# Optimization experiments

Hardware: AMD Instinct MI355X
Metric: run time of the kernel (lower is better)

Reference implementation:

```python
import jax, jax.numpy as jnp
import numpy as np

B, C, NQ, NK, S, H, FF = 8, 256, 1024, 4096, 16, 8, 2048
DH = C // H
EPS = 1e-5


def _layernorm(x, g, b):
    m = jnp.mean(x, axis=-1, keepdims=True)
    v = jnp.mean((x - m) ** 2, axis=-1, keepdims=True)
    return (x - m) * jax.lax.rsqrt(v + EPS) * g + b


def _box_query(key_pos, query_pos):
    # key_pos: (B,NK,3); query_pos: (B,NQ,6) = centers ++ box sizes (L,H,W)
    centers = query_pos[:, :, None, :3]            # (B,NQ,1,3)
    half = 0.5 * query_pos[:, :, None, 3:]         # (B,NQ,1,3)
    off = jnp.abs(key_pos[:, None, :, :] - centers)  # (B,NQ,NK,3)
    inside = jnp.all(off <= half, axis=-1)         # (B,NQ,NK)
    # first n_sample inside-points in index order (stable sort: inside first)
    order = jnp.argsort(~inside, axis=-1, stable=True)
    idx = order[..., :S]                           # (B,NQ,S)
    valid = jnp.take_along_axis(inside, idx, axis=-1)
    mask = ~valid                                  # True = padded / masked
    idx = jnp.where(mask, 0, idx)
    mask = mask.at[..., 0].set(False)              # matches cuda path: slot 0 never masked
    return idx, mask


def _forward(query, key, query_pos, key_pos,
             q_w, q_b, k_w, k_b, v_w, v_b, o_w, o_b,
             lin1_w, lin1_b, lin2_w, lin2_b,
             n1_g, n1_b, n2_g, n2_b, qpe_w, qpe_b, kpe_w, kpe_b):
    idx, mask = _box_query(key_pos, query_pos)     # (B,NQ,S), (B,NQ,S)
    # gather neighborhoods
    gxyz = jax.vmap(lambda kp, ix: kp[ix])(key_pos, idx)        # (B,NQ,S,3)
    gxyz = gxyz - query_pos[:, :, None, :3]                     # center-relative
    gfeat = jax.vmap(lambda kf, ix: kf[:, ix])(key, idx)        # (B,C,NQ,S)

    BQ = B * NQ
    kfeat = jnp.transpose(gfeat, (0, 2, 3, 1)).reshape(BQ, S, C)   # (BQ,S,C)
    kpe = gxyz.reshape(BQ, S, 3) @ kpe_w.T + kpe_b                 # cross_embed
    qtok = jnp.transpose(query, (0, 2, 1)).reshape(BQ, C)          # (BQ,C)
    qpe = (query_pos @ qpe_w.T + qpe_b).reshape(BQ, C)             # pos_embed

    # multihead cross-attention: 1 query vs S=16 local keys per group
    kv_in = kfeat + kpe
    qh = ((qtok + qpe) @ q_w.T + q_b).reshape(BQ, H, DH)
    kh = (kv_in @ k_w.T + k_b).reshape(BQ, S, H, DH)
    vh = (kv_in @ v_w.T + v_b).reshape(BQ, S, H, DH)
    scores = jnp.einsum('bhd,bshd->bhs', qh, kh) / np.sqrt(DH)    # (BQ,H,S)
    scores = jnp.where(mask.reshape(BQ, 1, S), -1e30, scores)
    attn = jax.nn.softmax(scores, axis=-1)
    ao = jnp.einsum('bhs,bshd->bhd', attn, vh).reshape(BQ, C)
    ao = ao @ o_w.T + o_b

    x = _layernorm(qtok + ao, n1_g, n1_b)                         # post-norm
    ff = jax.nn.relu(x @ lin1_w.T + lin1_b) @ lin2_w.T + lin2_b
    x = _layernorm(x + ff, n2_g, n2_b)
    return jnp.transpose(x.reshape(B, NQ, C), (0, 2, 1))          # (B,C,NQ)


def setup_inputs() -> dict:
    rng = jax.random.key(0)
    ks = jax.random.split(rng, 24)
    s = 0.02
    query = jax.random.normal(ks[0], (B, C, NQ), jnp.float32)
    key = jax.random.normal(ks[1], (B, C, NK), jnp.float32)
    key_pos = jax.random.uniform(ks[2], (B, NK, 3), jnp.float32)
    centers = jax.random.uniform(ks[3], (B, NQ, 3), jnp.float32)
    sizes = jax.random.uniform(ks[4], (B, NQ, 3), jnp.float32, minval=0.1, maxval=0.4)
    query_pos = jnp.concatenate([centers, sizes], axis=-1)
    p = {
        'q_w': jax.random.normal(ks[5], (C, C)) * s, 'q_b': jnp.zeros((C,)),
        'k_w': jax.random.normal(ks[6], (C, C)) * s, 'k_b': jnp.zeros((C,)),
        'v_w': jax.random.normal(ks[7], (C, C)) * s, 'v_b': jnp.zeros((C,)),
        'o_w': jax.random.normal(ks[8], (C, C)) * s, 'o_b': jnp.zeros((C,)),
        'lin1_w': jax.random.normal(ks[9], (FF, C)) * s, 'lin1_b': jnp.zeros((FF,)),
        'lin2_w': jax.random.normal(ks[10], (C, FF)) * s, 'lin2_b': jnp.zeros((C,)),
        'n1_g': jnp.ones((C,)), 'n1_b': jnp.zeros((C,)),
        'n2_g': jnp.ones((C,)), 'n2_b': jnp.zeros((C,)),
        'qpe_w': jax.random.normal(ks[11], (C, 6)) * s, 'qpe_b': jnp.zeros((C,)),
        'kpe_w': jax.random.normal(ks[12], (C, 3)) * s, 'kpe_b': jnp.zeros((C,)),
    }
    return dict(query=query, key=key, query_pos=query_pos, key_pos=key_pos, **p)


def reference(query, key, query_pos, key_pos,
              q_w, q_b, k_w, k_b, v_w, v_b, o_w, o_b,
              lin1_w, lin1_b, lin2_w, lin2_b,
              n1_g, n1_b, n2_g, n2_b, qpe_w, qpe_b, kpe_w, kpe_b):
    return _forward(query, key, query_pos, key_pos,
                    q_w, q_b, k_w, k_b, v_w, v_b, o_w, o_b,
                    lin1_w, lin1_b, lin2_w, lin2_b,
                    n1_g, n1_b, n2_g, n2_b, qpe_w, qpe_b, kpe_w, kpe_b)
```

## Files before the change

kernel.cpp:

```cpp
#include <hip/hip_runtime.h>
#include <cstdint>

#define B_   8
#define C_   256
#define NQ_  1024
#define NK_  4096
#define S_   16
#define H_   8
#define FF_  2048
#define DH_  32
#define BQ_  (B_*NQ_)
#define EPS_ 1e-5f

typedef __bf16 bf16x8 __attribute__((ext_vector_type(8)));
typedef __bf16 bf16x4 __attribute__((ext_vector_type(4)));
typedef float  f32x4  __attribute__((ext_vector_type(4)));

struct CvtArgs {
  const float* src[6];
  __bf16* dst[6];
};

__device__ __forceinline__ void gload_lds16(const void* g, void* l) {
  __builtin_amdgcn_global_load_lds(
      (const __attribute__((address_space(1))) void*)g,
      (__attribute__((address_space(3))) void*)l, 16, 0, 0);
}

#define SEGA 2048
#define SEGB 10240
#define SEGC 12288
#define SEGD 13568
#define NPREP 13584

__global__ __launch_bounds__(256) void k_prep(
    const float* __restrict__ query, const float* __restrict__ key,
    const float* __restrict__ query_pos, const float* __restrict__ key_pos,
    const float* __restrict__ qpe_w, const float* __restrict__ qpe_b,
    const float* __restrict__ k_w, const float* __restrict__ k_b,
    const float* __restrict__ v_w, const float* __restrict__ v_b,
    const float* __restrict__ kpe_w, const float* __restrict__ kpe_b,
    CvtArgs ca,
    __bf16* __restrict__ keyTb, __bf16* __restrict__ qtokb,
    __bf16* __restrict__ qinb,
    float4* __restrict__ Pk, float4* __restrict__ Pv,
    int* __restrict__ idxo, int* __restrict__ masko) {
  __shared__ __align__(16) float smem[1248];
  int blk = blockIdx.x, t = threadIdx.x;
  int tx = t & 31, ty = t >> 5;

  if (blk < SEGA) {
    int lane = t & 63;
    int q = blk * 4 + (t >> 6);
    int b = q >> 10;
    const float* kpb = key_pos + (size_t)b * NK_ * 3;
    const float* qp = query_pos + (size_t)q * 6;
    float cx = qp[0], cy = qp[1], cz = qp[2];
    float hx = 0.5f * qp[3], hy = 0.5f * qp[4], hz = 0.5f * qp[5];
    int* iq = idxo + (size_t)q * S_;
    int found = 0;
    for (int ch = 0; ch < NK_ / 64; ch += 4) {
      float dx[4], dy[4], dz[4];
#pragma unroll
      for (int u = 0; u < 4; ++u) {
        int k = (ch + u) * 64 + lane;
        dx[u] = fabsf(kpb[k * 3 + 0] - cx);
        dy[u] = fabsf(kpb[k * 3 + 1] - cy);
        dz[u] = fabsf(kpb[k * 3 + 2] - cz);
      }
#pragma unroll
      for (int u = 0; u < 4; ++u) {
        bool inside = (dx[u] <= hx) && (dy[u] <= hy) && (dz[u] <= hz);
        unsigned long long bal = __ballot(inside);
        if (inside) {
          int slot = found + __popcll(bal & ((1ull << lane) - 1ull));
          if (slot < S_) iq[slot] = (ch + u) * 64 + lane;
        }
        found += __popcll(bal);
      }
      if (found >= S_) break;
    }
    if (found > S_) found = S_;
    if (lane < S_) {
      int m = (lane < found) ? 0 : 1;
      if (lane >= found) iq[lane] = 0;
      if (lane == 0) m = 0;
      masko[(size_t)q * S_ + lane] = m;
    }
  } else if (blk < SEGB) {
    int local = blk - SEGA;
    float (*tt)[33] = (float(*)[33])smem;
    int x = local & 127, y = (local >> 7) & 7, z = local >> 10;
    int j0 = x * 32, i0 = y * 32;
    const float* inz = key + (size_t)z * C_ * NK_;
    __bf16* outz = keyTb + (size_t)z * NK_ * C_;
#pragma unroll
    for (int r = 0; r < 32; r += 8)
      tt[ty + r][tx] = inz[(size_t)(i0 + ty + r) * NK_ + (j0 + tx)];
    __syncthreads();
#pragma unroll
    for (int r = 0; r < 32; r += 8)
      outz[(size_t)(j0 + ty + r) * C_ + (i0 + tx)] = (__bf16)tt[tx][ty + r];
  } else if (blk < SEGC) {
    int local = blk - SEGB;
    float (*tt)[33] = (float(*)[33])smem;
    float (*sqp)[6] = (float(*)[6])(smem + 1056);
    int x = local & 31, y = (local >> 5) & 7, z = local >> 8;
    int nq0 = x * 32, c0 = y * 32;
    const float* inz = query + (size_t)z * C_ * NQ_;
#pragma unroll
    for (int r = 0; r < 32; r += 8)
      tt[ty + r][tx] = inz[(size_t)(c0 + ty + r) * NQ_ + (nq0 + tx)];
    if (t < 192)
      sqp[t / 6][t % 6] = query_pos[((size_t)z * NQ_ + nq0 + t / 6) * 6 + (t % 6)];
    int c = c0 + tx;
    float w0 = qpe_w[c * 6 + 0], w1 = qpe_w[c * 6 + 1], w2 = qpe_w[c * 6 + 2];
    float w3 = qpe_w[c * 6 + 3], w4 = qpe_w[c * 6 + 4], w5 = qpe_w[c * 6 + 5];
    float wb = qpe_b[c];
    __syncthreads();
#pragma unroll
    for (int r = 0; r < 32; r += 8) {
      int nql = ty + r;
      size_t row = (size_t)z * NQ_ + nq0 + nql;
      float v = tt[tx][nql];
      float pe = wb + sqp[nql][0] * w0 + sqp[nql][1] * w1 + sqp[nql][2] * w2 +
                 sqp[nql][3] * w3 + sqp[nql][4] * w4 + sqp[nql][5] * w5;
      qtokb[row * C_ + c] = (__bf16)v;
      qinb[row * C_ + c] = (__bf16)(v + pe);
    }
  } else if (blk < SEGD) {
    int local = blk - SEGC;
    int idx, base;
    if (local < 64)       { idx = 0; base = local; }
    else if (local < 128) { idx = 1; base = local - 64; }
    else if (local < 192) { idx = 2; base = local - 128; }
    else if (local < 256) { idx = 3; base = local - 192; }
    else if (local < 768) { idx = 4; base = local - 256; }
    else                  { idx = 5; base = local - 768; }
    size_t off = (size_t)base * 1024 + t * 4;
    float4 v = *(const float4*)(ca.src[idx] + off);
    __bf16* o = ca.dst[idx] + off;
    o[0] = (__bf16)v.x; o[1] = (__bf16)v.y; o[2] = (__bf16)v.z; o[3] = (__bf16)v.w;
  } else {
    int local = blk - SEGD;
    int bx = local & 7, bv = local >> 3;
    const float* w  = bv ? v_w : k_w;
    const float* wb = bv ? v_b : k_b;
    float4* P = bv ? Pv : Pk;
    float4 (*red)[8] = (float4(*)[8])smem;
    int nl = t >> 3, ks = (t & 7) * 32;
    int n = bx * 32 + nl;
    const float* wr = w + (size_t)n * C_;
    float p0 = 0.f, p1 = 0.f, p2 = 0.f, pb = 0.f;
#pragma unroll
    for (int k = ks; k < ks + 32; ++k) {
      float wv = wr[k];
      p0 += kpe_w[k * 3 + 0] * wv;
      p1 += kpe_w[k * 3 + 1] * wv;
      p2 += kpe_w[k * 3 + 2] * wv;
      pb += kpe_b[k] * wv;
    }
    red[nl][t & 7] = make_float4(p0, p1, p2, pb);
    __syncthreads();
    if (t < 32) {
      float4 s = red[t][0];
#pragma unroll
      for (int j = 1; j < 8; ++j) {
        float4 r = red[t][j];
        s.x += r.x; s.y += r.y; s.z += r.z; s.w += r.w;
      }
      s.w += wb[bx * 32 + t];
      P[bx * 32 + t] = s;
    }
  }
}

template <int BM, int BN>
__device__ __forceinline__ void gemm_tile(
    const __bf16* __restrict__ A, const __bf16* __restrict__ Wn,
    int m0, int n0, int K, int kbeg, int kend,
    __bf16 (*As)[64], __bf16 (*Bs)[64],
    f32x4 (&acc)[BM / 32][BN / 32]) {
  constexpr int MI = BM / 32, JN = BN / 32;
  constexpr int AI = BM / 32, BI = BN / 32;
  int t = threadIdx.x;
  int lane = t & 63, w = t >> 6;
  int lane16 = lane & 15, quad = lane >> 4;
  int wm = (w & 1) * (BM / 2), wn = (w >> 1) * (BN / 2);
  int l3 = lane >> 3;
  int lc = lane & 7;

  for (int k0 = kbeg; k0 < kend; k0 += 64) {
#pragma unroll
    for (int i = 0; i < AI; ++i) {
      int j = i * 4 + w;
      int row = j * 8 + l3;
      const __bf16* src = A + (size_t)(m0 + row) * K + k0 + ((lc ^ l3) << 3);
      gload_lds16(src, (char*)&As[0][0] + j * 1024);
    }
#pragma unroll
    for (int i = 0; i < BI; ++i) {
      int j = i * 4 + w;
      int row = j * 8 + l3;
      const __bf16* src = Wn + (size_t)(n0 + row) * K + k0 + ((lc ^ l3) << 3);
      gload_lds16(src, (char*)&Bs[0][0] + j * 1024);
    }
    __syncthreads();
#pragma unroll
    for (int kk = 0; kk < 64; kk += 32) {
      bf16x8 af[MI], bfr[JN];
      int qc = (kk >> 3) + quad;
#pragma unroll
      for (int i = 0; i < MI; ++i) {
        int row = wm + i * 16 + lane16;
        int ch = qc ^ (lane16 & 7);
        af[i] = *(const bf16x8*)((const char*)&As[row][0] + ch * 16);
      }
#pragma unroll
      for (int j = 0; j < JN; ++j) {
        int row = wn + j * 16 + lane16;
        int ch = qc ^ (lane16 & 7);
        bfr[j] = *(const bf16x8*)((const char*)&Bs[row][0] + ch * 16);
      }
#pragma unroll
      for (int i = 0; i < MI; ++i)
#pragma unroll
        for (int j = 0; j < JN; ++j)
          acc[i][j] = __builtin_amdgcn_mfma_f32_16x16x32_bf16(af[i], bfr[j], acc[i][j], 0, 0, 0);
    }
    __syncthreads();
  }
}

template <int BM, int BN, int RELU, int OUT_BF16>
__device__ __forceinline__ void gemm_body(
    const __bf16* __restrict__ A, const __bf16* __restrict__ Wn,
    const float* __restrict__ bias, void* __restrict__ outp,
    int n0, int m0, int N, int K, int kbeg, int kend) {
  constexpr int MI = BM / 32, JN = BN / 32;
  __shared__ __align__(16) __bf16 As[BM][64];
  __shared__ __align__(16) __bf16 Bs[BN][64];
  int t = threadIdx.x;
  int lane = t & 63, w = t >> 6;
  int lane16 = lane & 15, quad = lane >> 4;
  int wm = (w & 1) * (BM / 2), wn = (w >> 1) * (BN / 2);

  f32x4 acc[MI][JN];
#pragma unroll
  for (int i = 0; i < MI; ++i)
#pragma unroll
    for (int j = 0; j < JN; ++j) acc[i][j] = (f32x4){0.f, 0.f, 0.f, 0.f};

  gemm_tile<BM, BN>(A, Wn, m0, n0, K, kbeg, kend, As, Bs, acc);

#pragma unroll
  for (int j = 0; j < JN; ++j) {
    int col = n0 + wn + j * 16 + lane16;
    float bv = bias ? bias[col] : 0.f;
#pragma unroll
    for (int i = 0; i < MI; ++i) {
#pragma unroll
      for (int r = 0; r < 4; ++r) {
        int row = m0 + wm + i * 16 + quad * 4 + r;
        float v = acc[i][j][r] + bv;
        if (RELU) v = fmaxf(v, 0.f);
        if (OUT_BF16)
          ((__bf16*)outp)[(size_t)row * N + col] = (__bf16)v;
        else
          ((float*)outp)[(size_t)row * N + col] = v;
      }
    }
  }
}

template <int BM, int BN, int RELU, int OUT_BF16>
__global__ __launch_bounds__(256) void k_gemm(
    const __bf16* __restrict__ A, const __bf16* __restrict__ Wn,
    const float* __restrict__ bias, void* __restrict__ outp, int N, int K) {
  gemm_body<BM, BN, RELU, OUT_BF16>(A, Wn, bias, outp,
                                    blockIdx.x * BN, blockIdx.y * BM, N, K, 0, K);
}

__global__ __launch_bounds__(256) void k_gemm2(
    const __bf16* __restrict__ keyTb, const __bf16* __restrict__ kvwb,
    __bf16* __restrict__ khvbuf,
    const __bf16* __restrict__ qinb, const __bf16* __restrict__ qwb,
    const float* __restrict__ q_b, __bf16* __restrict__ qhb) {
  int blk = blockIdx.x;
  const __bf16 *A, *Wn; const float* bias; __bf16* outp; int n0, m0, N;
  if (blk < 1024) {
    A = keyTb; Wn = kvwb; bias = nullptr; outp = khvbuf;
    n0 = (blk & 3) * 128; m0 = (blk >> 2) * 128; N = 512;
  } else {
    int l = blk - 1024;
    A = qinb; Wn = qwb; bias = q_b; outp = qhb;
    n0 = (l & 1) * 128; m0 = (l >> 1) * 128; N = 256;
  }
  gemm_body<128, 128, 0, 1>(A, Wn, bias, outp, n0, m0, N, 256, 0, 256);
}

__global__ __launch_bounds__(256) void k_oln(
    const __bf16* __restrict__ A , const __bf16* __restrict__ Wn ,
    const float* __restrict__ obias, const __bf16* __restrict__ qtokb,
    const float* __restrict__ g, const float* __restrict__ bb,
    __bf16* __restrict__ x1b) {
  __shared__ __align__(16) __bf16 As[32][64];
  __shared__ __align__(16) __bf16 Bs[256][64];
  __shared__ float buf[32][257];
  int m0 = blockIdx.x * 32;
  int t = threadIdx.x;
  int lane = t & 63, w = t >> 6;
  int lane16 = lane & 15, quad = lane >> 4;
  int wm = (w & 1) * 16, wn = (w >> 1) * 128;

  f32x4 acc[1][8];
#pragma unroll
  for (int j = 0; j < 8; ++j) acc[0][j] = (f32x4){0.f, 0.f, 0.f, 0.f};
  gemm_tile<32, 256>(A, Wn, m0, 0, C_, 0, C_, As, Bs, acc);

#pragma unroll
  for (int j = 0; j < 8; ++j) {
    int col = wn + j * 16 + lane16;
    float bv = obias[col];
#pragma unroll
    for (int r = 0; r < 4; ++r)
      buf[wm + quad * 4 + r][col] = acc[0][j][r] + bv;
  }
  __syncthreads();

#pragma unroll
  for (int rr = 0; rr < 8; ++rr) {
    int row = w * 8 + rr;
    size_t grow = (size_t)(m0 + row);
    bf16x4 q4 = *(const bf16x4*)&qtokb[grow * C_ + lane * 4];
    float x0 = buf[row][lane * 4 + 0] + (float)q4[0];
    float x1 = buf[row][lane * 4 + 1] + (float)q4[1];
    float x2 = buf[row][lane * 4 + 2] + (float)q4[2];
    float x3 = buf[row][lane * 4 + 3] + (float)q4[3];
    float s = x0 + x1 + x2 + x3;
#pragma unroll
    for (int off = 32; off >= 1; off >>= 1) s += __shfl_xor(s, off);
    float mean = s * (1.f / C_);
    float d0 = x0 - mean, d1 = x1 - mean, d2 = x2 - mean, d3 = x3 - mean;
    float v = d0 * d0 + d1 * d1 + d2 * d2 + d3 * d3;
#pragma unroll
    for (int off = 32; off >= 1; off >>= 1) v += __shfl_xor(v, off);
    float inv = 1.f / sqrtf(v * (1.f / C_) + EPS_);
    float4 g4 = *(const float4*)(g + lane * 4);
    float4 b4 = *(const float4*)(bb + lane * 4);
    __bf16* obp = x1b + grow * C_ + lane * 4;
    obp[0] = (__bf16)(d0 * inv * g4.x + b4.x);
    obp[1] = (__bf16)(d1 * inv * g4.y + b4.y);
    obp[2] = (__bf16)(d2 * inv * g4.z + b4.z);
    obp[3] = (__bf16)(d3 * inv * g4.w + b4.w);
  }
}

__global__ __launch_bounds__(256) void k_ff2lnt(
    const __bf16* __restrict__ A , const __bf16* __restrict__ Wn ,
    const float* __restrict__ l2bias, const __bf16* __restrict__ x1b,
    const float* __restrict__ g, const float* __restrict__ bb,
    float* __restrict__ out) {
  __shared__ __align__(16) __bf16 As[32][64];
  __shared__ __align__(16) __bf16 Bs[256][64];
  __shared__ float buf[32][257];
  int m0 = blockIdx.x * 32;
  int t = threadIdx.x;
  int lane = t & 63, w = t >> 6;
  int lane16 = lane & 15, quad = lane >> 4;
  int wm = (w & 1) * 16, wn = (w >> 1) * 128;

  f32x4 acc[1][8];
#pragma unroll
  for (int j = 0; j < 8; ++j) acc[0][j] = (f32x4){0.f, 0.f, 0.f, 0.f};
  gemm_tile<32, 256>(A, Wn, m0, 0, FF_, 0, FF_, As, Bs, acc);

#pragma unroll
  for (int j = 0; j < 8; ++j) {
    int col = wn + j * 16 + lane16;
    float bv = l2bias[col];
#pragma unroll
    for (int r = 0; r < 4; ++r)
      buf[wm + quad * 4 + r][col] = acc[0][j][r] + bv;
  }
  __syncthreads();

  float4 g4 = *(const float4*)(g + lane * 4);
  float4 b4 = *(const float4*)(bb + lane * 4);
#pragma unroll
  for (int rr = 0; rr < 8; ++rr) {
    int row = w * 8 + rr;
    size_t grow = (size_t)(m0 + row);
    bf16x4 v4 = *(const bf16x4*)&x1b[grow * C_ + lane * 4];
    float x0 = buf[row][lane * 4 + 0] + (float)v4[0];
    float x1 = buf[row][lane * 4 + 1] + (float)v4[1];
    float x2 = buf[row][lane * 4 + 2] + (float)v4[2];
    float x3 = buf[row][lane * 4 + 3] + (float)v4[3];
    float s = x0 + x1 + x2 + x3;
#pragma unroll
    for (int off = 32; off >= 1; off >>= 1) s += __shfl_xor(s, off);
    float mean = s * (1.f / C_);
    float d0 = x0 - mean, d1 = x1 - mean, d2 = x2 - mean, d3 = x3 - mean;
    float v = d0 * d0 + d1 * d1 + d2 * d2 + d3 * d3;
#pragma unroll
    for (int off = 32; off >= 1; off >>= 1) v += __shfl_xor(v, off);
    float inv = 1.f / sqrtf(v * (1.f / C_) + EPS_);
    buf[row][lane * 4 + 0] = d0 * inv * g4.x + b4.x;
    buf[row][lane * 4 + 1] = d1 * inv * g4.y + b4.y;
    buf[row][lane * 4 + 2] = d2 * inv * g4.z + b4.z;
    buf[row][lane * 4 + 3] = d3 * inv * g4.w + b4.w;
  }
  __syncthreads();
  int z = m0 >> 10, nq0 = m0 & (NQ_ - 1);
  int tx = t & 31, ty = t >> 5;
#pragma unroll
  for (int ci = 0; ci < 32; ++ci) {
    int c = ci * 8 + ty;
    out[((size_t)z * C_ + c) * NQ_ + nq0 + tx] = buf[tx][c];
  }
}

__global__ __launch_bounds__(256) void k_attnf(
    const __bf16* __restrict__ khv,
    const float* __restrict__ key_pos,
    const float* __restrict__ query_pos,
    const int* __restrict__ idx,
    const int* __restrict__ maskb,
    const __bf16* __restrict__ qhb,
    const float4* __restrict__ Pk,
    const float4* __restrict__ Pv,
    __bf16* __restrict__ aob) {
  __shared__ __bf16 kvs[S_][520];
  __shared__ float qrow[C_];
  __shared__ float sc[H_][S_];
  __shared__ float pw[H_][S_];
  __shared__ float4 gx4[S_];
  __shared__ float4 pgxs[H_];
  __shared__ float4 qpks[H_];
  __shared__ int srow[S_], smask[S_];
  int bq = blockIdx.x, b = bq >> 10, t = threadIdx.x;

  if (t < S_) {
    int k = idx[(size_t)bq * S_ + t];
    srow[t] = b * NK_ + k;
    smask[t] = maskb[(size_t)bq * S_ + t];
    const float* kpp = key_pos + ((size_t)b * NK_ + k) * 3;
    const float* qp  = query_pos + (size_t)bq * 6;
    gx4[t] = make_float4(kpp[0] - qp[0], kpp[1] - qp[1], kpp[2] - qp[2], 1.f);
  }
  float qv_t = (float)qhb[(size_t)bq * C_ + t];
  qrow[t] = qv_t;
  {
    float4 p = Pk[t];
    p.x *= qv_t; p.y *= qv_t; p.z *= qv_t; p.w *= qv_t;
#pragma unroll
    for (int off = 16; off >= 1; off >>= 1) {
      p.x += __shfl_xor(p.x, off);
      p.y += __shfl_xor(p.y, off);
      p.z += __shfl_xor(p.z, off);
      p.w += __shfl_xor(p.w, off);
    }
    if ((t & 31) == 0) {
      const float s = 0.17677669529663687f;
      qpks[t >> 5] = make_float4(p.x * s, p.y * s, p.z * s, p.w * s);
    }
  }
  __syncthreads();
  {
    int s = t >> 4, c0 = (t & 15) * 32;
    const __bf16* src = khv + (size_t)srow[s] * 512 + c0;
    *(bf16x8*)&kvs[s][c0]      = *(const bf16x8*)&src[0];
    *(bf16x8*)&kvs[s][c0 + 8]  = *(const bf16x8*)&src[8];
    *(bf16x8*)&kvs[s][c0 + 16] = *(const bf16x8*)&src[16];
    *(bf16x8*)&kvs[s][c0 + 24] = *(const bf16x8*)&src[24];
  }
  __syncthreads();
  if (t < H_ * S_) {
    int h = t >> 4, s = t & (S_ - 1);
    float d = 0.f;
#pragma unroll
    for (int c0 = 0; c0 < 32; c0 += 8) {
      bf16x8 xv = *(const bf16x8*)&kvs[s][h * 32 + c0];
#pragma unroll
      for (int j = 0; j < 8; ++j) d += qrow[h * 32 + c0 + j] * (float)xv[j];
    }
    d *= 0.17677669529663687f;
    float4 g = gx4[s];
    float4 pk = qpks[h];
    d += g.x * pk.x + g.y * pk.y + g.z * pk.z + pk.w;
    if (smask[s]) d = -1e30f;
    sc[h][s] = d;
  }
  __syncthreads();
  if (t < H_) {
    float mx = -3.4e38f;
#pragma unroll
    for (int s = 0; s < S_; ++s) mx = fmaxf(mx, sc[t][s]);
    float e[S_], sum = 0.f;
#pragma unroll
    for (int s = 0; s < S_; ++s) { e[s] = expf(sc[t][s] - mx); sum += e[s]; }
    float inv = 1.f / sum;
    float gxx = 0.f, gyy = 0.f, gzz = 0.f;
#pragma unroll
    for (int s = 0; s < S_; ++s) {
      float p = e[s] * inv;
      pw[t][s] = p;
      float4 g = gx4[s];
      gxx += p * g.x; gyy += p * g.y; gzz += p * g.z;
    }
    pgxs[t] = make_float4(gxx, gyy, gzz, 1.f);
  }
  __syncthreads();
  {
    int h = t >> 5;
    float a = 0.f;
#pragma unroll
    for (int s = 0; s < S_; ++s) a += pw[h][s] * (float)kvs[s][256 + t];
    float4 pv = Pv[t];
    float4 g = pgxs[h];
    a += g.x * pv.x + g.y * pv.y + g.z * pv.z + pv.w;
    aob[(size_t)bq * C_ + t] = (__bf16)a;
  }
}

extern "C" void kernel_launch(void* const* d_in, const int* in_sizes, int n_in,
                              void* d_out, int out_size, void* d_ws, size_t ws_size,
                              hipStream_t stream) {
  const float* query     = (const float*)d_in[0];
  const float* key       = (const float*)d_in[1];
  const float* query_pos = (const float*)d_in[2];
  const float* key_pos   = (const float*)d_in[3];
  const float* q_w = (const float*)d_in[4];  const float* q_b = (const float*)d_in[5];
  const float* k_w = (const float*)d_in[6];  const float* k_b = (const float*)d_in[7];
  const float* v_w = (const float*)d_in[8];  const float* v_b = (const float*)d_in[9];
  const float* o_w = (const float*)d_in[10]; const float* o_b = (const float*)d_in[11];
  const float* lin1_w = (const float*)d_in[12]; const float* lin1_b = (const float*)d_in[13];
  const float* lin2_w = (const float*)d_in[14]; const float* lin2_b = (const float*)d_in[15];
  const float* n1_g = (const float*)d_in[16]; const float* n1_b = (const float*)d_in[17];
  const float* n2_g = (const float*)d_in[18]; const float* n2_b = (const float*)d_in[19];
  const float* qpe_w = (const float*)d_in[20]; const float* qpe_b = (const float*)d_in[21];
  const float* kpe_w = (const float*)d_in[22]; const float* kpe_b = (const float*)d_in[23];
  float* out = (float*)d_out;

  const size_t BQc = (size_t)BQ_ * C_;
  float* w = (float*)d_ws;
  size_t o = 0;
  __bf16* keyTb = (__bf16*)(w + o); o += (size_t)B_ * NK_ * C_ / 2;
  __bf16* qtokb = (__bf16*)(w + o); o += BQc / 2;
  __bf16* khvbuf = (__bf16*)(w + o); o += (size_t)B_ * NK_ * 512 / 2;
  __bf16* qinb = (__bf16*)(w + o); o += BQc / 2;
  __bf16* qhb  = (__bf16*)(w + o); o += BQc / 2;
  __bf16* aob  = (__bf16*)(w + o); o += BQc / 2;
  __bf16* x1b  = (__bf16*)(w + o); o += BQc / 2;
  __bf16* qwb  = (__bf16*)(w + o); o += (size_t)C_ * C_ / 2;
  __bf16* kvwb = (__bf16*)(w + o); o += (size_t)C_ * C_;
  __bf16* owb  = (__bf16*)(w + o); o += (size_t)C_ * C_ / 2;
  __bf16* l1b  = (__bf16*)(w + o); o += (size_t)C_ * FF_ / 2;
  __bf16* l2b  = (__bf16*)(w + o); o += (size_t)C_ * FF_ / 2;
  float4* Pk   = (float4*)(w + o); o += C_ * 4;
  float4* Pv   = (float4*)(w + o); o += C_ * 4;
  int* idxb  = (int*)(w + o); o += (size_t)BQ_ * S_;
  int* maskb = (int*)(w + o); o += (size_t)BQ_ * S_;
  __bf16* ff1b = khvbuf;

  CvtArgs ca;
  ca.src[0] = q_w; ca.dst[0] = qwb;
  ca.src[1] = k_w; ca.dst[1] = kvwb;
  ca.src[2] = v_w; ca.dst[2] = kvwb + (size_t)C_ * C_;
  ca.src[3] = o_w; ca.dst[3] = owb;
  ca.src[4] = lin1_w; ca.dst[4] = l1b;
  ca.src[5] = lin2_w; ca.dst[5] = l2b;
  k_prep<<<NPREP, 256, 0, stream>>>(query, key, query_pos, key_pos,
                                    qpe_w, qpe_b, k_w, k_b, v_w, v_b,
                                    kpe_w, kpe_b, ca,
                                    keyTb, qtokb, qinb, Pk, Pv, idxb, maskb);
  k_gemm2<<<1024 + 128, 256, 0, stream>>>(keyTb, kvwb, khvbuf, qinb, qwb, q_b, qhb);
  k_attnf<<<BQ_, 256, 0, stream>>>(khvbuf, key_pos, query_pos, idxb, maskb,
                                   qhb, Pk, Pv, aob);
  k_oln<<<BQ_ / 32, 256, 0, stream>>>(aob, owb, o_b, qtokb, n1_g, n1_b, x1b);
  k_gemm<128, 128, 1, 1><<<dim3(FF_ / 128, BQ_ / 128), 256, 0, stream>>>(
      x1b, l1b, lin1_b, ff1b, FF_, C_);
  k_ff2lnt<<<BQ_ / 32, 256, 0, stream>>>(ff1b, l2b, lin2_b, x1b, n2_g, n2_b, out);
}
```

Measured before the change: 258.4 us.

## Split K across two warp groups with double-buffered LDS in o-proj and FF2 kernels

Replaces the shared gemm_tile in the out-projection+LayerNorm and FF2+LayerNorm kernels with a new 512-thread GEMM. Two groups of four warps each handle half of K, with double-buffered async global-to-LDS loads and XOR-swizzled tiles, and the partial sums are combined through the shared buffer. The aim is more waves per tile to hide latency on the long-K FF2 GEMM (K=2048), and overlap of loads with MFMA. The cost is 144KB of LDS per block, which limits occupancy to one block per CU, plus an extra reduction pass with syncs.

```diff
diff --git a/kernel.cpp b/kernel.cpp
--- a/kernel.cpp
+++ b/kernel.cpp
@@ -299,38 +299,109 @@
   gemm_body<128, 128, 0, 1>(A, Wn, bias, outp, n0, m0, N, 256, 0, 256);
 }
 
-__global__ __launch_bounds__(256) void k_oln(
+template <int K>
+__device__ __forceinline__ void gemm32x256_sk2(
+    const __bf16* __restrict__ A, const __bf16* __restrict__ Wn,
+    const float* __restrict__ bias, int m0, char* smem, float (*buf)[257]) {
+  constexpr int NT = K / 2 / 64;
+  int t = threadIdx.x;
+  int lane = t & 63, w = t >> 6;
+  int kg = w >> 2, wl = w & 3;
+  int lane16 = lane & 15, quad = lane >> 4;
+  int wm = (wl & 1) * 16, wn = (wl >> 1) * 128;
+  int l3 = lane >> 3, lc = lane & 7;
+  int kbase = kg * (K / 2);
+
+  char* As0 = smem + kg * 8192;
+  char* Bs0 = smem + 16384 + kg * 65536;
+
+  f32x4 acc[8];
+#pragma unroll
+  for (int j = 0; j < 8; ++j) acc[j] = (f32x4){0.f, 0.f, 0.f, 0.f};
+
+  auto STAGE = [&](int bi, int ts) {
+    int k0 = kbase + ts * 64;
+    {
+      int j = wl;
+      int row = j * 8 + l3;
+      const __bf16* src = A + (size_t)(m0 + row) * K + k0 + ((lc ^ l3) << 3);
+      gload_lds16(src, As0 + bi * 4096 + j * 1024);
+    }
+#pragma unroll
+    for (int i = 0; i < 8; ++i) {
+      int j = i * 4 + wl;
+      int row = j * 8 + l3;
+      const __bf16* src = Wn + (size_t)row * K + k0 + ((lc ^ l3) << 3);
+      gload_lds16(src, Bs0 + bi * 32768 + j * 1024);
+    }
+  };
+
+  STAGE(0, 0);
+  __syncthreads();
+  int cur = 0;
+  for (int ts = 0; ts < NT; ++ts) {
+    if (ts + 1 < NT) STAGE(cur ^ 1, ts + 1);
+    const char* Ab = As0 + cur * 4096;
+    const char* Bb = Bs0 + cur * 32768;
+#pragma unroll
+    for (int kk = 0; kk < 64; kk += 32) {
+      int qc = (kk >> 3) + quad;
+      int ch = qc ^ (lane16 & 7);
+      bf16x8 af = *(const bf16x8*)(Ab + (wm + lane16) * 128 + ch * 16);
+      bf16x8 bfr[8];
+#pragma unroll
+      for (int j = 0; j < 8; ++j)
+        bfr[j] = *(const bf16x8*)(Bb + (wn + j * 16 + lane16) * 128 + ch * 16);
+#pragma unroll
+      for (int j = 0; j < 8; ++j)
+        acc[j] = __builtin_amdgcn_mfma_f32_16x16x32_bf16(af, bfr[j], acc[j], 0, 0, 0);
+    }
+    __syncthreads();
+    cur ^= 1;
+  }
+
+  if (kg == 1) {
+#pragma unroll
+    for (int j = 0; j < 8; ++j) {
+      int col = wn + j * 16 + lane16;
+#pragma unroll
+      for (int r = 0; r < 4; ++r)
+        buf[wm + quad * 4 + r][col] = acc[j][r];
+    }
+  }
+  __syncthreads();
+  if (kg == 0) {
+#pragma unroll
+    for (int j = 0; j < 8; ++j) {
+      int col = wn + j * 16 + lane16;
+      float bv = bias[col];
+#pragma unroll
+      for (int r = 0; r < 4; ++r) {
+        int row = wm + quad * 4 + r;
+        buf[row][col] += acc[j][r] + bv;
+      }
+    }
+  }
+  __syncthreads();
+}
+
+__global__ __launch_bounds__(512) void k_oln(
     const __bf16* __restrict__ A , const __bf16* __restrict__ Wn ,
     const float* __restrict__ obias, const __bf16* __restrict__ qtokb,
     const float* __restrict__ g, const float* __restrict__ bb,
     __bf16* __restrict__ x1b) {
-  __shared__ __align__(16) __bf16 As[32][64];
-  __shared__ __align__(16) __bf16 Bs[256][64];
-  __shared__ float buf[32][257];
+  __shared__ __align__(16) char smem[147456];
+  float (*buf)[257] = (float(*)[257])smem;
   int m0 = blockIdx.x * 32;
+  gemm32x256_sk2<C_>(A, Wn, obias, m0, smem, buf);
+
   int t = threadIdx.x;
   int lane = t & 63, w = t >> 6;
-  int lane16 = lane & 15, quad = lane >> 4;
-  int wm = (w & 1) * 16, wn = (w >> 1) * 128;
-
-  f32x4 acc[1][8];
-#pragma unroll
-  for (int j = 0; j < 8; ++j) acc[0][j] = (f32x4){0.f, 0.f, 0.f, 0.f};
-  gemm_tile<32, 256>(A, Wn, m0, 0, C_, 0, C_, As, Bs, acc);
-
-#pragma unroll
-  for (int j = 0; j < 8; ++j) {
-    int col = wn + j * 16 + lane16;
-    float bv = obias[col];
-#pragma unroll
-    for (int r = 0; r < 4; ++r)
-      buf[wm + quad * 4 + r][col] = acc[0][j][r] + bv;
-  }
-  __syncthreads();
-
-#pragma unroll
-  for (int rr = 0; rr < 8; ++rr) {
-    int row = w * 8 + rr;
+  float4 g4 = *(const float4*)(g + lane * 4);
+  float4 b4 = *(const float4*)(bb + lane * 4);
+#pragma unroll
+  for (int rr = 0; rr < 4; ++rr) {
+    int row = w * 4 + rr;
     size_t grow = (size_t)(m0 + row);
     bf16x4 q4 = *(const bf16x4*)&qtokb[grow * C_ + lane * 4];
     float x0 = buf[row][lane * 4 + 0] + (float)q4[0];
@@ -346,8 +417,6 @@
 #pragma unroll
     for (int off = 32; off >= 1; off >>= 1) v += __shfl_xor(v, off);
     float inv = 1.f / sqrtf(v * (1.f / C_) + EPS_);
-    float4 g4 = *(const float4*)(g + lane * 4);
-    float4 b4 = *(const float4*)(bb + lane * 4);
     __bf16* obp = x1b + grow * C_ + lane * 4;
     obp[0] = (__bf16)(d0 * inv * g4.x + b4.x);
     obp[1] = (__bf16)(d1 * inv * g4.y + b4.y);
@@ -356,40 +425,23 @@
   }
 }
 
-__global__ __launch_bounds__(256) void k_ff2lnt(
+__global__ __launch_bounds__(512) void k_ff2lnt(
     const __bf16* __restrict__ A , const __bf16* __restrict__ Wn ,
     const float* __restrict__ l2bias, const __bf16* __restrict__ x1b,
     const float* __restrict__ g, const float* __restrict__ bb,
     float* __restrict__ out) {
-  __shared__ __align__(16) __bf16 As[32][64];
-  __shared__ __align__(16) __bf16 Bs[256][64];
-  __shared__ float buf[32][257];
+  __shared__ __align__(16) char smem[147456];
+  float (*buf)[257] = (float(*)[257])smem;
   int m0 = blockIdx.x * 32;
+  gemm32x256_sk2<FF_>(A, Wn, l2bias, m0, smem, buf);
+
   int t = threadIdx.x;
   int lane = t & 63, w = t >> 6;
-  int lane16 = lane & 15, quad = lane >> 4;
-  int wm = (w & 1) * 16, wn = (w >> 1) * 128;
-
-  f32x4 acc[1][8];
-#pragma unroll
-  for (int j = 0; j < 8; ++j) acc[0][j] = (f32x4){0.f, 0.f, 0.f, 0.f};
-  gemm_tile<32, 256>(A, Wn, m0, 0, FF_, 0, FF_, As, Bs, acc);
-
-#pragma unroll
-  for (int j = 0; j < 8; ++j) {
-    int col = wn + j * 16 + lane16;
-    float bv = l2bias[col];
-#pragma unroll
-    for (int r = 0; r < 4; ++r)
-      buf[wm + quad * 4 + r][col] = acc[0][j][r] + bv;
-  }
-  __syncthreads();
-
   float4 g4 = *(const float4*)(g + lane * 4);
   float4 b4 = *(const float4*)(bb + lane * 4);
 #pragma unroll
-  for (int rr = 0; rr < 8; ++rr) {
-    int row = w * 8 + rr;
+  for (int rr = 0; rr < 4; ++rr) {
+    int row = w * 4 + rr;
     size_t grow = (size_t)(m0 + row);
     bf16x4 v4 = *(const bf16x4*)&x1b[grow * C_ + lane * 4];
     float x0 = buf[row][lane * 4 + 0] + (float)v4[0];
@@ -414,8 +466,8 @@
   int z = m0 >> 10, nq0 = m0 & (NQ_ - 1);
   int tx = t & 31, ty = t >> 5;
 #pragma unroll
-  for (int ci = 0; ci < 32; ++ci) {
-    int c = ci * 8 + ty;
+  for (int ci = 0; ci < 16; ++ci) {
+    int c = ci * 16 + ty;
     out[((size_t)z * C_ + c) * NQ_ + nq0 + tx] = buf[tx][c];
   }
 }
@@ -577,8 +629,8 @@
   k_gemm2<<<1024 + 128, 256, 0, stream>>>(keyTb, kvwb, khvbuf, qinb, qwb, q_b, qhb);
   k_attnf<<<BQ_, 256, 0, stream>>>(khvbuf, key_pos, query_pos, idxb, maskb,
                                    qhb, Pk, Pv, aob);
-  k_oln<<<BQ_ / 32, 256, 0, stream>>>(aob, owb, o_b, qtokb, n1_g, n1_b, x1b);
+  k_oln<<<BQ_ / 32, 512, 0, stream>>>(aob, owb, o_b, qtokb, n1_g, n1_b, x1b);
   k_gemm<128, 128, 1, 1><<<dim3(FF_ / 128, BQ_ / 128), 256, 0, stream>>>(
       x1b, l1b, lin1_b, ff1b, FF_, C_);
-  k_ff2lnt<<<BQ_ / 32, 256, 0, stream>>>(ff1b, l2b, lin2_b, x1b, n2_g, n2_b, out);
-}
+  k_ff2lnt<<<BQ_ / 32, 512, 0, stream>>>(ff1b, l2b, lin2_b, x1b, n2_g, n2_b, out);
+}
```

Result: faster. 246.7 us (-4.5%).
